# Kernel tuning notes

Hardware: AMD Instinct MI355X
Metric: run time of the kernel (lower is better)

The kernel has to match this reference:

```python
import jax, jax.numpy as jnp
import numpy as np
import math

LEVEL_DIMS = [256, 512, 1024, 2048]
B, P, K, D = 8192, 64, 8, 512
EPS = 1e-5  # torch LayerNorm default eps


def _layernorm(x, g, b):
    m = jnp.mean(x, axis=-1, keepdims=True)
    v = jnp.var(x, axis=-1, keepdims=True)
    return (x - m) / jnp.sqrt(v + EPS) * g + b


def _l2norm(x):
    # F.normalize(dim=-1): x / max(||x||_2, 1e-12)
    n = jnp.sqrt(jnp.sum(x * x, axis=-1, keepdims=True))
    return x / jnp.maximum(n, 1e-12)


def setup_inputs() -> dict:
    key = jax.random.key(0)
    ks = iter(jax.random.split(key, 32))
    inp = {}
    for i, dim in enumerate(LEVEL_DIMS):
        inp[f'pooled_{i}'] = jax.random.normal(next(ks), (B, dim), jnp.float32)
        inp[f'proto_{i}'] = jax.random.normal(next(ks), (P, dim), jnp.float32)
        inp[f'ln_g_{i}'] = jnp.ones((2 * dim,), jnp.float32)
        inp[f'ln_b_{i}'] = jnp.zeros((2 * dim,), jnp.float32)
        inp[f'W_{i}'] = jax.random.normal(next(ks), (2 * dim, D), jnp.float32) * (1.0 / math.sqrt(2 * dim))
        inp[f'b_{i}'] = jnp.zeros((D,), jnp.float32)
    inp['text_base'] = jax.random.normal(next(ks), (K, D), jnp.float32)
    inp['logit_scale'] = jnp.ones((1,), jnp.float32)
    return inp


def reference(pooled_0, pooled_1, pooled_2, pooled_3,
              proto_0, proto_1, proto_2, proto_3,
              ln_g_0, ln_g_1, ln_g_2, ln_g_3,
              ln_b_0, ln_b_1, ln_b_2, ln_b_3,
              W_0, W_1, W_2, W_3,
              b_0, b_1, b_2, b_3,
              text_base, logit_scale):
    pooled = [pooled_0, pooled_1, pooled_2, pooled_3]
    proto = [proto_0, proto_1, proto_2, proto_3]
    ln_g = [ln_g_0, ln_g_1, ln_g_2, ln_g_3]
    ln_b = [ln_b_0, ln_b_1, ln_b_2, ln_b_3]
    Ws = [W_0, W_1, W_2, W_3]
    bs = [b_0, b_1, b_2, b_3]

    # text encoder: CLIP embeddings normalized, text_proj=Identity, normalized again (idempotent)
    text_features = _l2norm(text_base)  # [K, D]

    ctxs = []
    for pl, pr, g, bb, W, b in zip(pooled, proto, ln_g, ln_b, Ws, bs):
        proto_ctx = jnp.broadcast_to(jnp.mean(pr, axis=0, keepdims=True), pl.shape)  # [B, C]
        fused = jnp.concatenate([pl, proto_ctx], axis=1)  # [B, 2C]
        h = jax.nn.relu(_layernorm(fused, g, bb) @ W + b)  # [B, D]
        ctxs.append(_l2norm(h))
    image_contexts = jnp.stack(ctxs, axis=1)  # [B, L, D]

    logits = jnp.einsum('kd,bld->bkl', text_features, image_contexts)
    logits = logits / math.sqrt(D)
    logits = logits * jnp.clip(logit_scale, 1e-4, None)
    return jax.nn.softmax(logits, axis=-1)  # [B, K, L]
```

## Files before the change

### kernel.cpp

```cpp
#include <hip/hip_runtime.h>
#include <stdint.h>

typedef __bf16 bf16x8 __attribute__((ext_vector_type(8)));
typedef float f32x4 __attribute__((ext_vector_type(4)));

#define OFF_ABF   0u
#define OFF_GWT   62914560u
#define OFF_H     66846720u
#define OFF_STAT  100401152u
#define OFF_TEXT  100663296u
#define OFF_U     100679680u
#define OFF_GG    100687872u
#define OFF_BB    100696064u
#define OFF_SCAL  100704256u
#define OFF_PMEAN 100704512u
#define WS_TOTAL  100719872u

__host__ __device__ __forceinline__ size_t abf_off(int l) {
  return (size_t)4194304u * (size_t)((1u << l) - 1u);
}
__host__ __device__ __forceinline__ size_t gwt_off(int l) {
  return (size_t)262144u * (size_t)((1u << l) - 1u);
}
__device__ __forceinline__ int pm_off(int l) { return 256 * ((1 << l) - 1); }

__device__ __forceinline__ unsigned short f2bf(float x) {
  return (unsigned short)((__float_as_uint(x) + 0x8000u) >> 16);
}
__device__ __forceinline__ unsigned pack2(float a, float b) {
  return ((__float_as_uint(a) + 0x8000u) >> 16) |
         ((__float_as_uint(b) + 0x8000u) & 0xffff0000u);
}
__device__ __forceinline__ void async_load16(const void* g, void* l) {
  __builtin_amdgcn_global_load_lds((const __attribute__((address_space(1))) void*)g,
                                   (__attribute__((address_space(3))) void*)l,
                                   16, 0, 0);
}

struct PrepArgs {
  const float* pooled[4];
  const float* proto[4];
  const float* W[4];
  const float* g[4];
  const float* beta[4];
  const float* bias[4];
  const float* text;
  const float* lsc;
  char* ws;
};


template <int R>
__device__ __forceinline__ void convProc(const char* ldsW, char* Dst, float* st,
                                         int rowBase, int lane) {
  constexpr int IPR = 8 / R;
#pragma unroll
  for (int r = 0; r < R; ++r) {
    float s1 = 0.f, s2 = 0.f;
#pragma unroll
    for (int p = 0; p < IPR; ++p) {
      int idx = lane + 64 * (r * IPR + p);
      const f32x4* src = (const f32x4*)(ldsW + 32 * (size_t)idx);
      f32x4 a = src[0], b = src[1];
      s1 += a[0] + a[1] + a[2] + a[3];
      s1 += b[0] + b[1] + b[2] + b[3];
      s2 = fmaf(a[0], a[0], s2); s2 = fmaf(a[1], a[1], s2);
      s2 = fmaf(a[2], a[2], s2); s2 = fmaf(a[3], a[3], s2);
      s2 = fmaf(b[0], b[0], s2); s2 = fmaf(b[1], b[1], s2);
      s2 = fmaf(b[2], b[2], s2); s2 = fmaf(b[3], b[3], s2);
      uint4 o = make_uint4(pack2(a[0], a[1]), pack2(a[2], a[3]),
                           pack2(b[0], b[1]), pack2(b[2], b[3]));
      *(uint4*)(Dst + 16 * (size_t)idx) = o;
    }
#pragma unroll
    for (int off = 1; off < 64; off <<= 1) {
      s1 += __shfl_xor(s1, off);
      s2 += __shfl_xor(s2, off);
    }
    if (lane == 0) {
      st[2 * (size_t)(rowBase + r)] = s1;
      st[2 * (size_t)(rowBase + r) + 1] = s2;
    }
  }
}

__device__ __forceinline__ void conv0(const char* ldsW, char* Dst, float* st,
                                      int rowBase, int lane) {
#pragma unroll
  for (int p = 0; p < 8; ++p) {
    int idx = lane + 64 * p;
    const f32x4* src = (const f32x4*)(ldsW + 32 * (size_t)idx);
    f32x4 a = src[0], b = src[1];
    float s1 = a[0] + a[1] + a[2] + a[3] + b[0] + b[1] + b[2] + b[3];
    float s2 = 0.f;
    s2 = fmaf(a[0], a[0], s2); s2 = fmaf(a[1], a[1], s2);
    s2 = fmaf(a[2], a[2], s2); s2 = fmaf(a[3], a[3], s2);
    s2 = fmaf(b[0], b[0], s2); s2 = fmaf(b[1], b[1], s2);
    s2 = fmaf(b[2], b[2], s2); s2 = fmaf(b[3], b[3], s2);
    uint4 o = make_uint4(pack2(a[0], a[1]), pack2(a[2], a[3]),
                         pack2(b[0], b[1]), pack2(b[2], b[3]));
    *(uint4*)(Dst + 16 * (size_t)idx) = o;
#pragma unroll
    for (int off = 1; off < 32; off <<= 1) {
      s1 += __shfl_xor(s1, off);
      s2 += __shfl_xor(s2, off);
    }
    if ((lane & 31) == 0) {
      int row = rowBase + 2 * p + (lane >> 5);
      st[2 * (size_t)row] = s1;
      st[2 * (size_t)row + 1] = s2;
    }
  }
}

__global__ __launch_bounds__(256, 2) void aconv(PrepArgs A) {
  __shared__ __align__(16) char sh[65536];
  int t = threadIdx.x, bid = blockIdx.x;
  int w = t >> 6, lane = t & 63;

  if (bid < 1920) {
    int g = bid * 4 + w;
    int l, rowBase;
    if (g < 4096)      { l = 3; rowBase = g * 2; }
    else if (g < 6144) { l = 2; rowBase = (g - 4096) * 4; }
    else if (g < 7168) { l = 1; rowBase = (g - 6144) * 8; }
    else               { l = 0; rowBase = (g - 7168) * 16; }
    int C = 256 << l;
    const float* P0 = A.pooled[l] + (size_t)rowBase * C;
    char* ldsW = sh + (w << 14);
#pragma unroll
    for (int i = 0; i < 16; ++i)
      async_load16(P0 + i * 256 + lane * 4, ldsW + (i << 10));
    asm volatile("s_waitcnt vmcnt(0)" ::: "memory");
    char* Dst = A.ws + OFF_ABF + abf_off(l) + (size_t)rowBase * C * 2;
    float* st = (float*)(A.ws + OFF_STAT) + (size_t)l * 8192 * 2;
    if (l == 3)      convProc<2>(ldsW, Dst, st, rowBase, lane);
    else if (l == 2) convProc<4>(ldsW, Dst, st, rowBase, lane);
    else if (l == 1) convProc<8>(ldsW, Dst, st, rowBase, lane);
    else             conv0(ldsW, Dst, st, rowBase, lane);
    return;
  }
  float(*redP)[64] = (float(*)[64])sh;
  float* scal = (float*)(A.ws + OFF_SCAL);
  if (bid < 1980) {
    int p = bid - 1920;
    int l, chunk;
    if (p < 32)      { l = 3; chunk = p; }
    else if (p < 48) { l = 2; chunk = p - 32; }
    else if (p < 56) { l = 1; chunk = p - 48; }
    else             { l = 0; chunk = p - 56; }
    int C = 256 << l;
    int c = chunk * 64 + lane;
    const float* pr = A.proto[l];
    float s = 0.f;
#pragma unroll
    for (int r = 0; r < 16; ++r) s += pr[(size_t)(w * 16 + r) * C + c];
    redP[w][lane] = s;
    __syncthreads();
    if (t < 64) {
      float pmv = (redP[0][t] + redP[1][t] + redP[2][t] + redP[3][t]) * (1.0f / 64.0f);
      ((float*)(A.ws + OFF_PMEAN))[pm_off(l) + chunk * 64 + t] = pmv;
      float s1 = pmv, s2 = pmv * pmv;
#pragma unroll
      for (int off = 1; off < 64; off <<= 1) {
        s1 += __shfl_xor(s1, off);
        s2 += __shfl_xor(s2, off);
      }
      if (t == 0) {
        atomicAdd(&scal[l], s1);
        atomicAdd(&scal[4 + l], s2);
      }
    }
    return;
  }
  float* r1 = &redP[0][0];
  float* tf = (float*)(A.ws + OFF_TEXT);
  for (int r = 0; r < 8; ++r) {
    float p = 0.f;
    for (int c = t; c < 512; c += 256) {
      float v = A.text[r * 512 + c];
      p += v * v;
    }
    r1[t] = p;
    __syncthreads();
    for (int o = 128; o > 0; o >>= 1) {
      if (t < o) r1[t] += r1[t + o];
      __syncthreads();
    }
    float inv = 1.0f / fmaxf(sqrtf(r1[0]), 1e-12f);
    __syncthreads();
    for (int c = t; c < 512; c += 256) tf[r * 512 + c] = A.text[r * 512 + c] * inv;
  }
  if (t == 0) {
    float s = fmaxf(A.lsc[0], 1e-4f);
    scal[8] = s * 0.04419417382415922f;
  }
}

__global__ __launch_bounds__(256) void wtrans(PrepArgs A) {
  __shared__ unsigned short tile[128][66];
  __shared__ float redG[4][128], redB[4][128], redU[4][128];
  __shared__ float gsh[64], bsh[64], psh[64];
  int t = threadIdx.x, bid = blockIdx.x;
  int l, idl;
  if (bid < 256)      { l = 3; idl = bid; }
  else if (bid < 384) { l = 2; idl = bid - 256; }
  else if (bid < 448) { l = 1; idl = bid - 384; }
  else                { l = 0; idl = bid - 448; }
  int C = 256 << l;
  int sid = idl >> 2, dchunk = idl & 3;
  int j0 = sid * 64, d0 = dchunk * 128;
  bool top = (j0 < C);

  if (t < 64) {
    float gv = A.g[l][j0 + t];
    gsh[t] = gv;
    bsh[t] = A.beta[l][j0 + t];
    if (!top)
      psh[t] = ((const float*)(A.ws + OFF_PMEAN))[pm_off(l) + (j0 - C) + t] * gv;
  }
  __syncthreads();

  int w = t >> 6, L = t & 63;
  const float* W = A.W[l];
  float2 v[16];
#pragma unroll
  for (int r = 0; r < 16; ++r) {
    int j = j0 + w * 16 + r;
    v[r] = *(const float2*)(W + (size_t)j * 512 + d0 + 2 * L);
  }
  float gp0 = 0.f, gp1 = 0.f, bp0 = 0.f, bp1 = 0.f, up0 = 0.f, up1 = 0.f;
#pragma unroll
  for (int r = 0; r < 16; ++r) {
    int jl = w * 16 + r;
    float g = gsh[jl], b = bsh[jl];
    gp0 = fmaf(g, v[r].x, gp0); gp1 = fmaf(g, v[r].y, gp1);
    bp0 = fmaf(b, v[r].x, bp0); bp1 = fmaf(b, v[r].y, bp1);
    if (top) {
      tile[2 * L][jl] = f2bf(g * v[r].x);
      tile[2 * L + 1][jl] = f2bf(g * v[r].y);
    } else {
      float p = psh[jl];
      up0 = fmaf(p, v[r].x, up0); up1 = fmaf(p, v[r].y, up1);
    }
  }
  redG[w][2 * L] = gp0; redG[w][2 * L + 1] = gp1;
  redB[w][2 * L] = bp0; redB[w][2 * L + 1] = bp1;
  if (!top) { redU[w][2 * L] = up0; redU[w][2 * L + 1] = up1; }
  __syncthreads();

  if (t < 128) {
    int d = l * 512 + d0 + t;
    float G = redG[0][t] + redG[1][t] + redG[2][t] + redG[3][t];
    float B = redB[0][t] + redB[1][t] + redB[2][t] + redB[3][t];
    atomicAdd(&((float*)(A.ws + OFF_GG))[d], G);
    atomicAdd(&((float*)(A.ws + OFF_BB))[d], B);
    if (!top) {
      float U = redU[0][t] + redU[1][t] + redU[2][t] + redU[3][t];
      atomicAdd(&((float*)(A.ws + OFF_U))[d], U);
    }
  }
  if (top) {
    unsigned short* gwT = (unsigned short*)(A.ws + OFF_GWT + gwt_off(l));
    int d = t >> 1, jh = (t & 1) * 32;
    const unsigned* trow = (const unsigned*)&tile[d][jh];
    uint4 q0 = make_uint4(trow[0], trow[1], trow[2], trow[3]);
    uint4 q1 = make_uint4(trow[4], trow[5], trow[6], trow[7]);
    uint4 q2 = make_uint4(trow[8], trow[9], trow[10], trow[11]);
    uint4 q3 = make_uint4(trow[12], trow[13], trow[14], trow[15]);
    uint4* dst = (uint4*)(gwT + (size_t)(d0 + d) * C + j0 + jh);
    dst[0] = q0; dst[1] = q1; dst[2] = q2; dst[3] = q3;
  }
}

struct G2Args {
  char* ws;
  const float* bias[4];
};

__global__ __launch_bounds__(256, 3) void gemm2(G2Args A) {
  __shared__ __align__(16) char lds[18944];
  char* ws = A.ws;
  int t = threadIdx.x, bid = blockIdx.x;
  int l = 3 - (bid >> 8);
  int rb = (bid >> 2) & 63, cb = bid & 3;
  int C = 256 << l;
  int m0 = rb * 128, n0 = cb * 128;

  float* uArr  = (float*)(lds + 16384);
  float* gArr  = (float*)(lds + 16896);
  float* bArr  = (float*)(lds + 17408);
  float* rowM  = (float*)(lds + 17920);
  float* rowIS = (float*)(lds + 18432);
  const float* scal = (const float*)(ws + OFF_SCAL);

  if (t < 128) {
    int idx = l * 512 + n0 + t;
    uArr[t] = ((const float*)(ws + OFF_U))[idx];
    gArr[t] = ((const float*)(ws + OFF_GG))[idx];
    bArr[t] = ((const float*)(ws + OFF_BB))[idx] + A.bias[l][n0 + t];
  } else {
    int r = t - 128;
    const float* st = (const float*)(ws + OFF_STAT) + (size_t)(l * 8192 + m0 + r) * 2;
    float s1 = st[0], s2 = st[1];
    float inv2C = 1.0f / (float)(2 * C);
    float mr = (s1 + scal[l]) * inv2C;
    float var = (s2 + scal[4 + l]) * inv2C - mr * mr;
    rowM[r] = mr;
    rowIS[r] = rsqrtf(var + 1e-5f);
  }

  int w = t >> 6, lane = t & 63, quad = lane >> 4, lc = lane & 15;
  const char* Abf = ws + OFF_ABF + abf_off(l);
  const char* Bw  = ws + OFF_GWT + gwt_off(l);
  const char* aP[2]; const char* bP[2];
  char* aD[2]; char* bD[2];
#pragma unroll
  for (int i = 0; i < 2; ++i) {
    int li = i * 256 + t;
    int rr = li >> 2, kq = li & 3;
    aP[i] = Abf + ((size_t)(m0 + rr) * C + kq * 8) * 2;
    bP[i] = Bw  + ((size_t)(n0 + rr) * C + kq * 8) * 2;
    aD[i] = lds + i * 4096 + w * 1024;
    bD[i] = lds + 8192 + i * 4096 + w * 1024;
  }
  int wr = (w >> 1) * 64, wc = (w & 1) * 64;
  const char* aF = lds + (wr + lc) * 64 + quad * 16;
  const char* bF = lds + 8192 + (wc + lc) * 64 + quad * 16;

  f32x4 acc[4][4] = {};
  for (int k0 = 0; k0 < C; k0 += 32) {
    async_load16(aP[0], aD[0]); async_load16(aP[1], aD[1]);
    async_load16(bP[0], bD[0]); async_load16(bP[1], bD[1]);
    aP[0] += 64; aP[1] += 64; bP[0] += 64; bP[1] += 64;
    __syncthreads();
    bf16x8 av[4];
#pragma unroll
    for (int rt = 0; rt < 4; ++rt) av[rt] = *(const bf16x8*)(aF + rt * 1024);
#pragma unroll
    for (int ct = 0; ct < 4; ++ct) {
      bf16x8 bv = *(const bf16x8*)(bF + ct * 1024);
#pragma unroll
      for (int rt = 0; rt < 4; ++rt)
        acc[rt][ct] = __builtin_amdgcn_mfma_f32_16x16x32_bf16(av[rt], bv, acc[rt][ct], 0, 0, 0);
    }
    __syncthreads();
  }

  char* Hl = ws + OFF_H + (size_t)l * 8388608;
#pragma unroll
  for (int rt = 0; rt < 4; ++rt) {
#pragma unroll
    for (int ct = 0; ct < 4; ++ct) {
      int nl = wc + ct * 16 + lc;
      float uu = uArr[nl], gg = gArr[nl], bb = bArr[nl];
      f32x4 a = acc[rt][ct];
#pragma unroll
      for (int reg = 0; reg < 4; ++reg) {
        int ml = wr + rt * 16 + quad * 4 + reg;
        float h = fmaf(a[reg] + uu - rowM[ml] * gg, rowIS[ml], bb);
        h = fmaxf(h, 0.f);
        float hp = __shfl_xor(h, 1);
        if (!(lc & 1)) {
          unsigned pkv = pack2(h, hp);
          *(unsigned*)(Hl + ((size_t)(m0 + ml) * 512 + n0 + nl) * 2) = pkv;
        }
      }
    }
  }
}

__global__ __launch_bounds__(256) void postK(const char* ws, float* out) {
  __shared__ float textL[4096];
  int t = threadIdx.x, b = blockIdx.x;
  const float* tf = (const float*)(ws + OFF_TEXT);
  for (int i = t; i < 4096; i += 256) textL[i] = tf[i];
  __syncthreads();
  float scale = ((const float*)(ws + OFF_SCAL))[8];
  int row = b * 16 + (t >> 4), q = t & 15;
  float lg[4][8];
#pragma unroll
  for (int l = 0; l < 4; ++l) {
    const uint4* hp = (const uint4*)(ws + OFF_H + (size_t)l * 8388608 +
                                     ((size_t)row * 512 + q * 32) * 2);
    float np = 0.f;
    float dp[8] = {};
#pragma unroll
    for (int ch = 0; ch < 4; ++ch) {
      uint4 u = hp[ch];
      int d0 = q * 32 + ch * 8;
      unsigned uw[4] = {u.x, u.y, u.z, u.w};
#pragma unroll
      for (int p = 0; p < 4; ++p) {
        float v0 = __uint_as_float(uw[p] << 16);
        float v1 = __uint_as_float(uw[p] & 0xffff0000u);
        int dd = d0 + p * 2;
        np = fmaf(v0, v0, np);
        np = fmaf(v1, v1, np);
#pragma unroll
        for (int k = 0; k < 8; ++k) {
          dp[k] = fmaf(v0, textL[k * 512 + dd], dp[k]);
          dp[k] = fmaf(v1, textL[k * 512 + dd + 1], dp[k]);
        }
      }
    }
#pragma unroll
    for (int off = 1; off < 16; off <<= 1) {
      np += __shfl_xor(np, off);
#pragma unroll
      for (int k = 0; k < 8; ++k) dp[k] += __shfl_xor(dp[k], off);
    }
    float innorm = scale / fmaxf(sqrtf(np), 1e-12f);
#pragma unroll
    for (int k = 0; k < 8; ++k) lg[l][k] = dp[k] * innorm;
  }
  if (q == 0) {
    float4* op = (float4*)out + (size_t)row * 8;
#pragma unroll
    for (int k = 0; k < 8; ++k) {
      float a = lg[0][k], b2 = lg[1][k], c = lg[2][k], d = lg[3][k];
      float mx = fmaxf(fmaxf(a, b2), fmaxf(c, d));
      float e0 = __expf(a - mx), e1 = __expf(b2 - mx);
      float e2 = __expf(c - mx), e3 = __expf(d - mx);
      float inv = 1.0f / (e0 + e1 + e2 + e3);
      op[k] = make_float4(e0 * inv, e1 * inv, e2 * inv, e3 * inv);
    }
  }
}

extern "C" void kernel_launch(void* const* d_in, const int* in_sizes, int n_in,
                              void* d_out, int out_size, void* d_ws, size_t ws_size,
                              hipStream_t stream) {
  (void)n_in; (void)out_size;
  if (ws_size < (size_t)WS_TOTAL) return;
  char* ws = (char*)d_ws;
  bool dict = (in_sizes[1] == 64 * 256);
  PrepArgs pa;
  for (int l = 0; l < 4; ++l) {
    if (dict) {
      pa.pooled[l] = (const float*)d_in[6 * l + 0];
      pa.proto[l]  = (const float*)d_in[6 * l + 1];
      pa.g[l]      = (const float*)d_in[6 * l + 2];
      pa.beta[l]   = (const float*)d_in[6 * l + 3];
      pa.W[l]      = (const float*)d_in[6 * l + 4];
      pa.bias[l]   = (const float*)d_in[6 * l + 5];
    } else {
      pa.pooled[l] = (const float*)d_in[l];
      pa.proto[l]  = (const float*)d_in[4 + l];
      pa.g[l]      = (const float*)d_in[8 + l];
      pa.beta[l]   = (const float*)d_in[12 + l];
      pa.W[l]      = (const float*)d_in[16 + l];
      pa.bias[l]   = (const float*)d_in[20 + l];
    }
  }
  pa.text = (const float*)d_in[24];
  pa.lsc = (const float*)d_in[25];
  pa.ws = ws;

  hipMemsetAsync(ws + OFF_U, 0, 3 * 8192 + 256, stream);
  aconv<<<1981, 256, 0, stream>>>(pa);
  wtrans<<<480, 256, 0, stream>>>(pa);

  G2Args g2;
  g2.ws = ws;
  for (int l = 0; l < 4; ++l) g2.bias[l] = pa.bias[l];
  gemm2<<<1024, 256, 0, stream>>>(g2);
  postK<<<512, 256, 0, stream>>>(ws, (float*)d_out);
}
```

Baseline: 299.1 us.

## Replace LDS-staged fp32-to-bf16 conversion with register double-buffered persistent waves

The activation conversion kernel no longer stages each wave's rows through 64KB of shared memory with async LDS loads. Each wave now handles eight 8KB units, loading the next unit into registers while it converts and reduces the current one, and the grid shrinks from 1981 to 541 blocks. Occupancy rises to four blocks per SM via launch bounds because shared memory use drops to a small reduction buffer. The aim is to overlap global loads with conversion and cut LDS traffic and launch overhead, at the cost of higher register pressure and fewer, longer-lived waves.

```diff
diff --git a/kernel.cpp b/kernel.cpp
--- a/kernel.cpp
+++ b/kernel.cpp
@@ -50,100 +50,123 @@
 };
 
 
+__device__ __forceinline__ void loadUnit(f32x4 (&buf)[8], const f32x4* base, int lane) {
+#pragma unroll
+  for (int i = 0; i < 4; ++i) {
+    buf[2 * i]     = base[2 * (lane + 64 * i)];
+    buf[2 * i + 1] = base[2 * (lane + 64 * i) + 1];
+  }
+}
+
 template <int R>
-__device__ __forceinline__ void convProc(const char* ldsW, char* Dst, float* st,
+__device__ __forceinline__ void procUnit(const f32x4 (&v)[8], char* Dst, float* st,
                                          int rowBase, int lane) {
-  constexpr int IPR = 8 / R;
-#pragma unroll
-  for (int r = 0; r < R; ++r) {
-    float s1 = 0.f, s2 = 0.f;
-#pragma unroll
-    for (int p = 0; p < IPR; ++p) {
-      int idx = lane + 64 * (r * IPR + p);
-      const f32x4* src = (const f32x4*)(ldsW + 32 * (size_t)idx);
-      f32x4 a = src[0], b = src[1];
-      s1 += a[0] + a[1] + a[2] + a[3];
-      s1 += b[0] + b[1] + b[2] + b[3];
-      s2 = fmaf(a[0], a[0], s2); s2 = fmaf(a[1], a[1], s2);
-      s2 = fmaf(a[2], a[2], s2); s2 = fmaf(a[3], a[3], s2);
-      s2 = fmaf(b[0], b[0], s2); s2 = fmaf(b[1], b[1], s2);
-      s2 = fmaf(b[2], b[2], s2); s2 = fmaf(b[3], b[3], s2);
-      uint4 o = make_uint4(pack2(a[0], a[1]), pack2(a[2], a[3]),
-                           pack2(b[0], b[1]), pack2(b[2], b[3]));
-      *(uint4*)(Dst + 16 * (size_t)idx) = o;
-    }
-#pragma unroll
-    for (int off = 1; off < 64; off <<= 1) {
-      s1 += __shfl_xor(s1, off);
-      s2 += __shfl_xor(s2, off);
-    }
-    if (lane == 0) {
-      st[2 * (size_t)(rowBase + r)] = s1;
-      st[2 * (size_t)(rowBase + r) + 1] = s2;
-    }
-  }
-}
-
-__device__ __forceinline__ void conv0(const char* ldsW, char* Dst, float* st,
-                                      int rowBase, int lane) {
-#pragma unroll
-  for (int p = 0; p < 8; ++p) {
-    int idx = lane + 64 * p;
-    const f32x4* src = (const f32x4*)(ldsW + 32 * (size_t)idx);
-    f32x4 a = src[0], b = src[1];
-    float s1 = a[0] + a[1] + a[2] + a[3] + b[0] + b[1] + b[2] + b[3];
+  float p1[4], p2[4];
+#pragma unroll
+  for (int i = 0; i < 4; ++i) {
+    f32x4 a = v[2 * i], b = v[2 * i + 1];
+    float s1 = ((a[0] + a[1]) + (a[2] + a[3])) + ((b[0] + b[1]) + (b[2] + b[3]));
     float s2 = 0.f;
     s2 = fmaf(a[0], a[0], s2); s2 = fmaf(a[1], a[1], s2);
     s2 = fmaf(a[2], a[2], s2); s2 = fmaf(a[3], a[3], s2);
     s2 = fmaf(b[0], b[0], s2); s2 = fmaf(b[1], b[1], s2);
     s2 = fmaf(b[2], b[2], s2); s2 = fmaf(b[3], b[3], s2);
+    p1[i] = s1; p2[i] = s2;
     uint4 o = make_uint4(pack2(a[0], a[1]), pack2(a[2], a[3]),
                          pack2(b[0], b[1]), pack2(b[2], b[3]));
-    *(uint4*)(Dst + 16 * (size_t)idx) = o;
-#pragma unroll
-    for (int off = 1; off < 32; off <<= 1) {
-      s1 += __shfl_xor(s1, off);
-      s2 += __shfl_xor(s2, off);
-    }
-    if ((lane & 31) == 0) {
-      int row = rowBase + 2 * p + (lane >> 5);
-      st[2 * (size_t)row] = s1;
-      st[2 * (size_t)row + 1] = s2;
-    }
-  }
-}
-
-__global__ __launch_bounds__(256, 2) void aconv(PrepArgs A) {
-  __shared__ __align__(16) char sh[65536];
+    *(uint4*)(Dst + 16 * (size_t)(lane + 64 * i)) = o;
+  }
+  if constexpr (R == 1) {
+    float s1 = (p1[0] + p1[1]) + (p1[2] + p1[3]);
+    float s2 = (p2[0] + p2[1]) + (p2[2] + p2[3]);
+#pragma unroll
+    for (int off = 1; off < 64; off <<= 1) {
+      s1 += __shfl_xor(s1, off); s2 += __shfl_xor(s2, off);
+    }
+    if (lane == 0) {
+      st[2 * (size_t)rowBase] = s1; st[2 * (size_t)rowBase + 1] = s2;
+    }
+  } else if constexpr (R == 2) {
+#pragma unroll
+    for (int h = 0; h < 2; ++h) {
+      float s1 = p1[2 * h] + p1[2 * h + 1], s2 = p2[2 * h] + p2[2 * h + 1];
+#pragma unroll
+      for (int off = 1; off < 64; off <<= 1) {
+        s1 += __shfl_xor(s1, off); s2 += __shfl_xor(s2, off);
+      }
+      if (lane == 0) {
+        st[2 * (size_t)(rowBase + h)] = s1; st[2 * (size_t)(rowBase + h) + 1] = s2;
+      }
+    }
+  } else if constexpr (R == 4) {
+#pragma unroll
+    for (int i = 0; i < 4; ++i) {
+      float s1 = p1[i], s2 = p2[i];
+#pragma unroll
+      for (int off = 1; off < 64; off <<= 1) {
+        s1 += __shfl_xor(s1, off); s2 += __shfl_xor(s2, off);
+      }
+      if (lane == 0) {
+        st[2 * (size_t)(rowBase + i)] = s1; st[2 * (size_t)(rowBase + i) + 1] = s2;
+      }
+    }
+  } else {
+#pragma unroll
+    for (int i = 0; i < 4; ++i) {
+      float s1 = p1[i], s2 = p2[i];
+#pragma unroll
+      for (int off = 1; off < 32; off <<= 1) {
+        s1 += __shfl_xor(s1, off); s2 += __shfl_xor(s2, off);
+      }
+      if ((lane & 31) == 0) {
+        int row = rowBase + 2 * i + (lane >> 5);
+        st[2 * (size_t)row] = s1; st[2 * (size_t)row + 1] = s2;
+      }
+    }
+  }
+}
+
+template <int R>
+__device__ __forceinline__ void waveRun(const f32x4* P, char* Dst, float* st,
+                                        int rowBase, int lane) {
+  f32x4 bufA[8], bufB[8];
+  loadUnit(bufA, P, lane);
+#pragma unroll
+  for (int k = 0; k < 8; ++k) {
+    if ((k & 1) == 0) {
+      if (k < 7) loadUnit(bufB, P + (size_t)(k + 1) * 512, lane);
+      procUnit<R>(bufA, Dst + (size_t)k * 4096, st, rowBase + k * R, lane);
+    } else {
+      if (k < 7) loadUnit(bufA, P + (size_t)(k + 1) * 512, lane);
+      procUnit<R>(bufB, Dst + (size_t)k * 4096, st, rowBase + k * R, lane);
+    }
+  }
+}
+
+__global__ __launch_bounds__(256, 4) void aconv(PrepArgs A) {
+  __shared__ float redP[4][64];
   int t = threadIdx.x, bid = blockIdx.x;
   int w = t >> 6, lane = t & 63;
 
-  if (bid < 1920) {
-    int g = bid * 4 + w;
-    int l, rowBase;
-    if (g < 4096)      { l = 3; rowBase = g * 2; }
-    else if (g < 6144) { l = 2; rowBase = (g - 4096) * 4; }
-    else if (g < 7168) { l = 1; rowBase = (g - 6144) * 8; }
-    else               { l = 0; rowBase = (g - 7168) * 16; }
-    int C = 256 << l;
-    const float* P0 = A.pooled[l] + (size_t)rowBase * C;
-    char* ldsW = sh + (w << 14);
-#pragma unroll
-    for (int i = 0; i < 16; ++i)
-      async_load16(P0 + i * 256 + lane * 4, ldsW + (i << 10));
-    asm volatile("s_waitcnt vmcnt(0)" ::: "memory");
-    char* Dst = A.ws + OFF_ABF + abf_off(l) + (size_t)rowBase * C * 2;
+  if (bid < 480) {
+    int u0 = (bid * 4 + w) * 8;
+    int l, uL;
+    if (u0 < 8192)       { l = 3; uL = u0; }
+    else if (u0 < 12288) { l = 2; uL = u0 - 8192; }
+    else if (u0 < 14336) { l = 1; uL = u0 - 12288; }
+    else                 { l = 0; uL = u0 - 14336; }
+    const f32x4* P = (const f32x4*)A.pooled[l] + (size_t)uL * 512;
+    char* Dst = A.ws + OFF_ABF + abf_off(l) + (size_t)uL * 4096;
     float* st = (float*)(A.ws + OFF_STAT) + (size_t)l * 8192 * 2;
-    if (l == 3)      convProc<2>(ldsW, Dst, st, rowBase, lane);
-    else if (l == 2) convProc<4>(ldsW, Dst, st, rowBase, lane);
-    else if (l == 1) convProc<8>(ldsW, Dst, st, rowBase, lane);
-    else             conv0(ldsW, Dst, st, rowBase, lane);
+    if (l == 3)      waveRun<1>(P, Dst, st, uL,     lane);
+    else if (l == 2) waveRun<2>(P, Dst, st, uL * 2, lane);
+    else if (l == 1) waveRun<4>(P, Dst, st, uL * 4, lane);
+    else             waveRun<8>(P, Dst, st, uL * 8, lane);
     return;
   }
-  float(*redP)[64] = (float(*)[64])sh;
   float* scal = (float*)(A.ws + OFF_SCAL);
-  if (bid < 1980) {
-    int p = bid - 1920;
+  if (bid < 540) {
+    int p = bid - 480;
     int l, chunk;
     if (p < 32)      { l = 3; chunk = p; }
     else if (p < 48) { l = 2; chunk = p - 32; }
@@ -458,7 +481,7 @@
   pa.ws = ws;
 
   hipMemsetAsync(ws + OFF_U, 0, 3 * 8192 + 256, stream);
-  aconv<<<1981, 256, 0, stream>>>(pa);
+  aconv<<<541, 256, 0, stream>>>(pa);
   wtrans<<<480, 256, 0, stream>>>(pa);
 
   G2Args g2;
```

New measurement: 299.8 us. Within noise of the previous version (+0.2%).
